# Kernel tuning notes

Hardware: AMD Instinct MI355X
Metric: run time of the kernel (lower is better)

The kernel has to match this reference:

```python
import jax, jax.numpy as jnp
import numpy as np

N, E = 50000, 800000
IN, HID, HEADS = 64, 32, 4


def setup_inputs() -> dict:
    key = jax.random.key(0)
    ks = jax.random.split(key, 18)
    x = jax.random.normal(ks[0], (N, IN), jnp.float32)
    edge_index = jax.random.randint(ks[1], (2, E), 0, N)

    def lin(k, fan_in, fan_out):
        kw, kb = jax.random.split(k)
        bound = 1.0 / np.sqrt(fan_in)
        W = jax.random.uniform(kw, (fan_in, fan_out), jnp.float32, -bound, bound)
        b = jax.random.uniform(kb, (fan_out,), jnp.float32, -bound, bound)
        return W, b

    # layer 1: in=IN, out=HID per head, heads=HEADS, concat=True -> out dim HID*HEADS
    Wq1, bq1 = lin(ks[2], IN, HEADS * HID)
    Wk1, bk1 = lin(ks[3], IN, HEADS * HID)
    Wv1, bv1 = lin(ks[4], IN, HEADS * HID)
    Ws1, bs1 = lin(ks[5], IN, HEADS * HID)  # root/skip lin
    # layer 2: in=HID*HEADS, out=HID, heads=1, concat=False
    IN2 = HID * HEADS
    Wq2, bq2 = lin(ks[6], IN2, HID)
    Wk2, bk2 = lin(ks[7], IN2, HID)
    Wv2, bv2 = lin(ks[8], IN2, HID)
    Ws2, bs2 = lin(ks[9], IN2, HID)
    return dict(x=x, edge_index=edge_index,
                Wq1=Wq1, bq1=bq1, Wk1=Wk1, bk1=bk1, Wv1=Wv1, bv1=bv1, Ws1=Ws1, bs1=bs1,
                Wq2=Wq2, bq2=bq2, Wk2=Wk2, bk2=bk2, Wv2=Wv2, bv2=bv2, Ws2=Ws2, bs2=bs2)


def transformer_conv(x, src, dst, Wq, bq, Wk, bk, Wv, bv, Ws, bs, heads, out_ch, concat):
    """PyG TransformerConv (eval mode, root_weight=True, beta=False)."""
    n = x.shape[0]
    q = (x @ Wq + bq).reshape(n, heads, out_ch)  # [N,H,C]
    k = (x @ Wk + bk).reshape(n, heads, out_ch)
    v = (x @ Wv + bv).reshape(n, heads, out_ch)
    # per-edge attention logits: q_i . k_j / sqrt(C)
    logits = jnp.einsum('ehc,ehc->eh', q[dst], k[src]) / jnp.sqrt(jnp.float32(out_ch))
    # segment softmax over incoming edges of each target node
    m = jax.ops.segment_max(logits, dst, num_segments=n)          # [N,H]
    p = jnp.exp(logits - m[dst])                                   # [E,H]
    denom = jax.ops.segment_sum(p, dst, num_segments=n)            # [N,H]
    alpha = p / denom[dst]                                         # [E,H]
    agg = jax.ops.segment_sum(alpha[:, :, None] * v[src], dst, num_segments=n)  # [N,H,C]
    if concat:
        o = agg.reshape(n, heads * out_ch)
    else:
        o = agg.mean(axis=1)
    return o + x @ Ws + bs


def reference(x, edge_index,
              Wq1, bq1, Wk1, bk1, Wv1, bv1, Ws1, bs1,
              Wq2, bq2, Wk2, bk2, Wv2, bv2, Ws2, bs2):
    src, dst = edge_index[0], edge_index[1]
    h = transformer_conv(x, src, dst, Wq1, bq1, Wk1, bk1, Wv1, bv1, Ws1, bs1,
                         HEADS, HID, True)
    h = jax.nn.elu(h)
    out = transformer_conv(h, src, dst, Wq2, bq2, Wk2, bk2, Wv2, bv2, Ws2, bs2,
                           1, HID, False)
    return out
```

## Files before the change

### kernel.cpp

```cpp
#include <hip/hip_runtime.h>
#include <hip/hip_bf16.h>
#include <hip/hip_fp8.h>

#define N_NODES 50000
#define N_EDGES 800000
#define HB 3125
#define GB1 1563
#define NBS 49

static constexpr float SCALE = 0.17677669529663687f;

typedef __attribute__((ext_vector_type(8))) short bf16x8;
typedef __attribute__((ext_vector_type(4))) float f32x4;
typedef __attribute__((ext_vector_type(2))) float f32x2;
#define MFMA16 __builtin_amdgcn_mfma_f32_16x16x32_bf16
#define CVT8 __builtin_amdgcn_cvt_pk_f32_fp8

static __device__ inline unsigned short f2bf(float f) {
    __hip_bfloat16 h = __float2bfloat16(f);
    return __builtin_bit_cast(unsigned short, h);
}
static __device__ inline unsigned char f2fp8(float f) {
    __hip_fp8_e4m3 h(f);
    return __builtin_bit_cast(unsigned char, h);
}
static __device__ inline f32x2 bfp2(unsigned u) {
    f32x2 r;
    r[0] = __uint_as_float(u << 16);
    r[1] = __uint_as_float(u & 0xffff0000u);
    return r;
}


__global__ __launch_bounds__(256) void k_wf(
    const float* __restrict__ Wq1, const float* __restrict__ Wk1,
    const float* __restrict__ Wv1, const float* __restrict__ Ws1,
    const float* __restrict__ Wq2, const float* __restrict__ Wk2,
    const float* __restrict__ Wv2, const float* __restrict__ Ws2,
    unsigned short* __restrict__ Wf1, unsigned short* __restrict__ Wf2,
    int* __restrict__ cnt)
{
    int id = blockIdx.x * 256 + threadIdx.x;
    if (id < N_NODES + 64) cnt[id] = 0;
    if (id < 32768) {
        int j = id & 7, l = (id >> 3) & 63, ks = (id >> 9) & 1, nt = (id >> 10) & 7, m = (id >> 13) & 3;
        const float* W = (m == 0) ? Wq1 : (m == 1) ? Wk1 : (m == 2) ? Wv1 : Ws1;
        int k = ks * 32 + ((l >> 4) << 3) + j;
        int c = nt * 16 + (l & 15);
        Wf1[id] = f2bf(W[k * 128 + c]);
    } else if (id < 49152) {
        int id2 = id - 32768;
        int j = id2 & 7, l = (id2 >> 3) & 63, ks = (id2 >> 9) & 3, g = (id2 >> 11) & 7;
        int m = g >> 1, t = g & 1;
        const float* W = (m == 0) ? Wq2 : (m == 1) ? Wk2 : (m == 2) ? Wv2 : Ws2;
        int k = ks * 32 + ((l >> 4) << 3) + j;
        int c = t * 16 + (l & 15);
        Wf2[id2] = f2bf(W[k * 32 + c]);
    }
}


__global__ __launch_bounds__(256) void k_hg(
    const int* __restrict__ dst, int* __restrict__ cnt, int* __restrict__ rank,
    const float* __restrict__ x, const unsigned short* __restrict__ Wf1,
    const float* __restrict__ bq, const float* __restrict__ bk,
    const float* __restrict__ bv, const float* __restrict__ bs,
    unsigned short* __restrict__ qs1, unsigned char* __restrict__ kv8, int n)
{
    __shared__ unsigned char smem[4 * 4352];
    if (blockIdx.x < HB) {
        int e = blockIdx.x * 256 + threadIdx.x;
        rank[e] = atomicAdd(&cnt[dst[e]], 1);
        return;
    }
    int w = threadIdx.x >> 6;
    int l = threadIdx.x & 63;
    int rb = (blockIdx.x - HB) * 32;
    int lr = l & 15, lk = l >> 4;
    unsigned short* xs = (unsigned short*)smem;
    {
        int t = threadIdx.x;
        int r = rb + (t >> 3);
        if (r >= n) r = n - 1;
        int c = (t & 7) * 8;
        const float* xp = x + (size_t)r * 64 + c;
        float4 f0 = *(const float4*)xp;
        float4 f1 = *(const float4*)(xp + 4);
        unsigned short* dp = xs + (t >> 3) * 72 + c;
        dp[0] = f2bf(f0.x); dp[1] = f2bf(f0.y); dp[2] = f2bf(f0.z); dp[3] = f2bf(f0.w);
        dp[4] = f2bf(f1.x); dp[5] = f2bf(f1.y); dp[6] = f2bf(f1.z); dp[7] = f2bf(f1.w);
    }
    __syncthreads();
    f32x4 acc[2][8];
#pragma unroll
    for (int mt = 0; mt < 2; ++mt)
#pragma unroll
        for (int nt = 0; nt < 8; ++nt) acc[mt][nt] = (f32x4){0.f, 0.f, 0.f, 0.f};
#pragma unroll
    for (int ks = 0; ks < 2; ++ks) {
        bf16x8 a[2];
#pragma unroll
        for (int mt = 0; mt < 2; ++mt)
            a[mt] = *(const bf16x8*)(xs + (mt * 16 + lr) * 72 + ks * 32 + lk * 8);
#pragma unroll
        for (int nt = 0; nt < 8; ++nt) {
            bf16x8 b = *(const bf16x8*)(Wf1 + (size_t)((w * 8 + nt) * 1024 + ks * 512 + l * 8));
            acc[0][nt] = MFMA16(a[0], b, acc[0][nt], 0, 0, 0);
            acc[1][nt] = MFMA16(a[1], b, acc[1][nt], 0, 0, 0);
        }
    }
    __syncthreads();
    const float* bptr = (w == 0) ? bq : (w == 1) ? bk : (w == 2) ? bv : bs;
    unsigned char* my = smem + w * 4352;
#pragma unroll
    for (int mt = 0; mt < 2; ++mt) {
        if (w == 1 || w == 2) {
            unsigned char* lb = my;
#pragma unroll
            for (int nt = 0; nt < 8; ++nt) {
                float bias = bptr[nt * 16 + lr];
#pragma unroll
                for (int i = 0; i < 4; ++i)
                    lb[(lk * 4 + i) * 144 + nt * 16 + lr] = f2fp8(acc[mt][nt][i] + bias);
            }
            int voff = (w == 2) ? 8 : 0;
#pragma unroll
            for (int p = 0; p < 4; ++p) {
                int rl = p * 4 + lk;
                int r = rb + mt * 16 + rl;
                if (r < n) {
                    uint2 val = *(const uint2*)(lb + rl * 144 + lr * 8);
                    *(uint2*)(kv8 + (size_t)r * 256 + lr * 16 + voff) = val;
                }
            }
        } else {
            unsigned short* ls = (unsigned short*)my;
#pragma unroll
            for (int nt = 0; nt < 8; ++nt) {
                float bias = bptr[nt * 16 + lr];
#pragma unroll
                for (int i = 0; i < 4; ++i)
                    ls[(lk * 4 + i) * 136 + nt * 16 + lr] = f2bf(acc[mt][nt][i] + bias);
            }
            unsigned short* outp = (w == 0) ? qs1 : qs1 + 128;
#pragma unroll
            for (int p = 0; p < 4; ++p) {
                int rl = p * 4 + lk;
                int r = rb + mt * 16 + rl;
                if (r < n) {
                    uint4 val = *(const uint4*)(ls + rl * 136 + lr * 8);
                    *(uint4*)(outp + (size_t)r * 256 + lr * 8) = val;
                }
            }
        }
    }
}


__global__ __launch_bounds__(256) void k_scan(const int* __restrict__ cnt,
                                              int* __restrict__ row,
                                              int* __restrict__ bsum,
                                              int* __restrict__ boff,
                                              int* __restrict__ ctr, int n) {
    __shared__ int wsum[4];
    __shared__ int lastBlk;
    int t = threadIdx.x;
    int base = blockIdx.x * 1024 + t * 4;
    int v0 = (base + 0 < n) ? cnt[base + 0] : 0;
    int v1i = (base + 1 < n) ? cnt[base + 1] : 0;
    int v2 = (base + 2 < n) ? cnt[base + 2] : 0;
    int v3 = (base + 3 < n) ? cnt[base + 3] : 0;
    int s = v0 + v1i + v2 + v3;
    int lane = t & 63, wid = t >> 6;
    int sc = s;
#pragma unroll
    for (int d = 1; d < 64; d <<= 1) {
        int o = __shfl_up(sc, d);
        if (lane >= d) sc += o;
    }
    if (lane == 63) wsum[wid] = sc;
    __syncthreads();
    int woff = 0;
    for (int w = 0; w < wid; ++w) woff += wsum[w];
    int excl = woff + sc - s;
    if (base + 0 < n) row[base + 0] = excl;
    if (base + 1 < n) row[base + 1] = excl + v0;
    if (base + 2 < n) row[base + 2] = excl + v0 + v1i;
    if (base + 3 < n) row[base + 3] = excl + v0 + v1i + v2;
    if (t == 255) {
        bsum[blockIdx.x] = woff + sc;
        __threadfence();
        lastBlk = (atomicAdd(ctr, 1) == NBS - 1);
    }
    __syncthreads();
    if (lastBlk && t < 64) {
        __threadfence();
        int v = (t < NBS) ? ((volatile int*)bsum)[t] : 0;
        int sc2 = v;
#pragma unroll
        for (int d = 1; d < 64; d <<= 1) {
            int o = __shfl_up(sc2, d);
            if (t >= d) sc2 += o;
        }
        boff[t] = sc2 - v;
        if (t == (N_NODES >> 10)) row[N_NODES] = N_EDGES - (sc2 - v);
    }
}


__global__ void k_scat(const int* __restrict__ src, const int* __restrict__ dst,
                       const int* __restrict__ row, const int* __restrict__ boff,
                       const int* __restrict__ rank, int* __restrict__ col) {
    int e = blockIdx.x * 256 + threadIdx.x;
    int de = dst[e];
    col[row[de] + boff[de >> 10] + rank[e]] = src[e];
}


__global__ __launch_bounds__(256) void k_gemm2m(
    const unsigned short* __restrict__ h1b, const unsigned short* __restrict__ Wf2,
    const float* __restrict__ bq, const float* __restrict__ bk,
    const float* __restrict__ bv, const float* __restrict__ bs,
    unsigned short* __restrict__ qs2, unsigned char* __restrict__ k82,
    unsigned short* __restrict__ v2, int n)
{
    __shared__ unsigned short lds[4][32][72];
    int w = threadIdx.x >> 6;
    int l = threadIdx.x & 63;
    int half = w & 1;
    int rb = blockIdx.x * 64 + (w >> 1) * 32;
    int lr = l & 15, lk = l >> 4;
    f32x4 acc[2][4];
#pragma unroll
    for (int mt = 0; mt < 2; ++mt)
#pragma unroll
        for (int nt = 0; nt < 4; ++nt) acc[mt][nt] = (f32x4){0.f, 0.f, 0.f, 0.f};
#pragma unroll
    for (int ks = 0; ks < 4; ++ks) {
        bf16x8 a[2];
#pragma unroll
        for (int mt = 0; mt < 2; ++mt) {
            int r = rb + mt * 16 + lr;
            if (r >= n) r = n - 1;
            a[mt] = *(const bf16x8*)(h1b + (size_t)r * 128 + ks * 32 + lk * 8);
        }
#pragma unroll
        for (int nt = 0; nt < 4; ++nt) {
            int g = half * 4 + nt;
            bf16x8 b = *(const bf16x8*)(Wf2 + (size_t)((g * 4 + ks) * 512 + l * 8));
            acc[0][nt] = MFMA16(a[0], b, acc[0][nt], 0, 0, 0);
            acc[1][nt] = MFMA16(a[1], b, acc[1][nt], 0, 0, 0);
        }
    }
#pragma unroll
    for (int nt = 0; nt < 4; ++nt) {
        int g = half * 4 + nt;
        int mat = g >> 1;
        int c = (g * 16 + lr) & 31;
        const float* bp = (mat == 0) ? bq : (mat == 1) ? bk : (mat == 2) ? bv : bs;
        float bias = bp[c];
#pragma unroll
        for (int mt = 0; mt < 2; ++mt)
#pragma unroll
            for (int i = 0; i < 4; ++i)
                lds[w][mt * 16 + lk * 4 + i][nt * 16 + lr] = f2bf(acc[mt][nt][i] + bias);
    }
    int rl8 = l >> 3, ci = (l & 7) * 4;
#pragma unroll
    for (int p = 0; p < 4; ++p) {
        int rl = p * 8 + rl8;
        int r = rb + rl;
        if (r < n) {
            uint2 va = *(const uint2*)&lds[w][rl][ci];
            uint2 vb = *(const uint2*)&lds[w][rl][32 + ci];
            if (half == 0) {
                *(uint2*)(qs2 + (size_t)r * 64 + ci) = va;
                unsigned pk =
                      (unsigned)f2fp8(__uint_as_float(vb.x << 16))
                    | ((unsigned)f2fp8(__uint_as_float(vb.x & 0xffff0000u)) << 8)
                    | ((unsigned)f2fp8(__uint_as_float(vb.y << 16)) << 16)
                    | ((unsigned)f2fp8(__uint_as_float(vb.y & 0xffff0000u)) << 24);
                *(unsigned*)(k82 + (size_t)r * 32 + ci) = pk;
            } else {
                *(uint2*)(v2 + (size_t)r * 32 + ci) = va;
                *(uint2*)(qs2 + (size_t)r * 64 + 32 + ci) = vb;
            }
        }
    }
}


__global__ __launch_bounds__(256) void k_agg1(
    const unsigned short* __restrict__ qs1, const unsigned char* __restrict__ kv8,
    const int* __restrict__ row, const int* __restrict__ boff,
    const int* __restrict__ col, uint4* __restrict__ h1b, int n)
{
    int i = blockIdx.x * 4 + (threadIdx.x >> 6);
    if (i >= n) return;
    int lane = threadIdx.x & 63;
    int slot = lane >> 4, w = lane & 15;
    f32x2 q2[4];
    {
        uint4 qu = *(const uint4*)(qs1 + (size_t)i * 256 + w * 8);
        q2[0] = bfp2(qu.x); q2[1] = bfp2(qu.y); q2[2] = bfp2(qu.z); q2[3] = bfp2(qu.w);
    }
    f32x2 acc2[4] = {};
    float d = 0.f;
    int s = row[i] + boff[i >> 10];
    int e = row[i + 1] + boff[(i + 1) >> 10];
    for (int t = s; t < e; t += 8) {
        int ta = t + slot, tb = t + 4 + slot;
        bool va = ta < e, vb = tb < e;
        int ja = col[va ? ta : s];
        int jb = col[vb ? tb : s];
        uint4 A = *(const uint4*)(kv8 + (size_t)ja * 256 + w * 16);
        uint4 B = *(const uint4*)(kv8 + (size_t)jb * 256 + w * 16);
        f32x2 pa = CVT8(A.x, false) * q2[0];
        pa += CVT8(A.x, true)  * q2[1];
        pa += CVT8(A.y, false) * q2[2];
        pa += CVT8(A.y, true)  * q2[3];
        f32x2 pb = CVT8(B.x, false) * q2[0];
        pb += CVT8(B.x, true)  * q2[1];
        pb += CVT8(B.y, false) * q2[2];
        pb += CVT8(B.y, true)  * q2[3];
        float la = pa[0] + pa[1];
        float lb = pb[0] + pb[1];
        la += __shfl_xor(la, 1);  lb += __shfl_xor(lb, 1);
        la += __shfl_xor(la, 2);  lb += __shfl_xor(lb, 2);
        float wa = va ? __expf(la * SCALE) : 0.f;
        float wb = vb ? __expf(lb * SCALE) : 0.f;
        d += wa + wb;
        f32x2 wa2 = (f32x2){wa, wa};
        f32x2 wb2 = (f32x2){wb, wb};
        acc2[0] += wa2 * CVT8(A.z, false);
        acc2[1] += wa2 * CVT8(A.z, true);
        acc2[2] += wa2 * CVT8(A.w, false);
        acc2[3] += wa2 * CVT8(A.w, true);
        acc2[0] += wb2 * CVT8(B.z, false);
        acc2[1] += wb2 * CVT8(B.z, true);
        acc2[2] += wb2 * CVT8(B.w, false);
        acc2[3] += wb2 * CVT8(B.w, true);
    }
    float acc[8] = {acc2[0][0], acc2[0][1], acc2[1][0], acc2[1][1],
                    acc2[2][0], acc2[2][1], acc2[3][0], acc2[3][1]};
#pragma unroll
    for (int m = 16; m <= 32; m <<= 1) {
        d += __shfl_xor(d, m);
#pragma unroll
        for (int c = 0; c < 8; ++c) acc[c] += __shfl_xor(acc[c], m);
    }
    if (slot == 0) {
        float inv = (d > 0.f) ? 1.f / d : 0.f;
        uint4 su = *(const uint4*)(qs1 + (size_t)i * 256 + 128 + w * 8);
        f32x2 sv[4] = {bfp2(su.x), bfp2(su.y), bfp2(su.z), bfp2(su.w)};
        unsigned o[4];
#pragma unroll
        for (int p = 0; p < 4; ++p) {
            float rx = acc[2 * p] * inv + sv[p][0];
            float ry = acc[2 * p + 1] * inv + sv[p][1];
            rx = (rx > 0.f) ? rx : expm1f(rx);
            ry = (ry > 0.f) ? ry : expm1f(ry);
            o[p] = ((unsigned)f2bf(ry) << 16) | (unsigned)f2bf(rx);
        }
        h1b[(size_t)i * 16 + w] = make_uint4(o[0], o[1], o[2], o[3]);
    }
}


__global__ __launch_bounds__(256) void k_agg2(
    const unsigned short* __restrict__ qs2, const unsigned char* __restrict__ k82,
    const unsigned short* __restrict__ v2,
    const int* __restrict__ row, const int* __restrict__ boff,
    const int* __restrict__ col, float* __restrict__ out, int n)
{
    int i = blockIdx.x * 4 + (threadIdx.x >> 6);
    if (i >= n) return;
    int lane = threadIdx.x & 63;
    int slot = lane >> 2, qr = lane & 3;
    f32x2 q2[4];
    {
        uint4 qu = *(const uint4*)(qs2 + (size_t)i * 64 + qr * 8);
        q2[0] = bfp2(qu.x); q2[1] = bfp2(qu.y); q2[2] = bfp2(qu.z); q2[3] = bfp2(qu.w);
    }
    f32x2 acc2[4] = {};
    float d = 0.f;
    int s = row[i] + boff[i >> 10];
    int e = row[i + 1] + boff[(i + 1) >> 10];
    for (int t = s; t < e; t += 16) {
        int te = t + slot;
        bool va = te < e;
        int j = col[va ? te : s];
        uint2 ku = *(const uint2*)(k82 + (size_t)j * 32 + qr * 8);
        uint4 vu = *(const uint4*)(v2 + (size_t)j * 32 + qr * 8);
        f32x2 pp = CVT8(ku.x, false) * q2[0];
        pp += CVT8(ku.x, true)  * q2[1];
        pp += CVT8(ku.y, false) * q2[2];
        pp += CVT8(ku.y, true)  * q2[3];
        float lg = pp[0] + pp[1];
        lg += __shfl_xor(lg, 1);
        lg += __shfl_xor(lg, 2);
        float wv = va ? __expf(lg * SCALE) : 0.f;
        d += wv;
        f32x2 w2 = (f32x2){wv, wv};
        acc2[0] += w2 * bfp2(vu.x);
        acc2[1] += w2 * bfp2(vu.y);
        acc2[2] += w2 * bfp2(vu.z);
        acc2[3] += w2 * bfp2(vu.w);
    }
    float acc[8] = {acc2[0][0], acc2[0][1], acc2[1][0], acc2[1][1],
                    acc2[2][0], acc2[2][1], acc2[3][0], acc2[3][1]};
#pragma unroll
    for (int m = 4; m <= 32; m <<= 1) {
        d += __shfl_xor(d, m);
#pragma unroll
        for (int c = 0; c < 8; ++c) acc[c] += __shfl_xor(acc[c], m);
    }
    if (slot == 0) {
        float inv = (d > 0.f) ? 1.f / d : 0.f;
        uint4 su = *(const uint4*)(qs2 + (size_t)i * 64 + 32 + qr * 8);
        f32x2 sv[4] = {bfp2(su.x), bfp2(su.y), bfp2(su.z), bfp2(su.w)};
        float4 o0, o1;
        o0.x = acc[0] * inv + sv[0][0];
        o0.y = acc[1] * inv + sv[0][1];
        o0.z = acc[2] * inv + sv[1][0];
        o0.w = acc[3] * inv + sv[1][1];
        o1.x = acc[4] * inv + sv[2][0];
        o1.y = acc[5] * inv + sv[2][1];
        o1.z = acc[6] * inv + sv[3][0];
        o1.w = acc[7] * inv + sv[3][1];
        *(float4*)&out[(size_t)i * 32 + qr * 8] = o0;
        *(float4*)&out[(size_t)i * 32 + qr * 8 + 4] = o1;
    }
}


extern "C" void kernel_launch(void* const* d_in, const int* in_sizes, int n_in,
                              void* d_out, int out_size, void* d_ws, size_t ws_size,
                              hipStream_t stream)
{
    const int N = N_NODES, E = N_EDGES;
    const float* x   = (const float*)d_in[0];
    const int* edge  = (const int*)d_in[1];
    const int* src   = edge;
    const int* dst   = edge + E;
    const float* Wq1 = (const float*)d_in[2];  const float* bq1 = (const float*)d_in[3];
    const float* Wk1 = (const float*)d_in[4];  const float* bk1 = (const float*)d_in[5];
    const float* Wv1 = (const float*)d_in[6];  const float* bv1 = (const float*)d_in[7];
    const float* Ws1 = (const float*)d_in[8];  const float* bs1 = (const float*)d_in[9];
    const float* Wq2 = (const float*)d_in[10]; const float* bq2 = (const float*)d_in[11];
    const float* Wk2 = (const float*)d_in[12]; const float* bk2 = (const float*)d_in[13];
    const float* Wv2 = (const float*)d_in[14]; const float* bv2 = (const float*)d_in[15];
    const float* Ws2 = (const float*)d_in[16]; const float* bs2 = (const float*)d_in[17];

    char* ws = (char*)d_ws;
    size_t off = 0;
    auto alloc = [&](size_t bytes) -> void* {
        void* p = ws + off;
        off += (bytes + 255) & ~(size_t)255;
        return p;
    };
    unsigned short* qs1 = (unsigned short*)alloc((size_t)N * 256 * 2);
    unsigned char*  kv8 = (unsigned char*)alloc((size_t)N * 256);
    unsigned short* h1b = (unsigned short*)alloc((size_t)N * 128 * 2);
    unsigned short* qs2 = (unsigned short*)alloc((size_t)N * 64 * 2);
    unsigned char*  k82 = (unsigned char*)alloc((size_t)N * 32);
    unsigned short* v2  = (unsigned short*)alloc((size_t)N * 32 * 2);
    unsigned short* Wf1 = (unsigned short*)alloc(32768 * 2);
    unsigned short* Wf2 = (unsigned short*)alloc(16384 * 2);
    int* row_ptr  = (int*)alloc((size_t)(N + 1) * 4);
    int* cnt      = (int*)alloc((size_t)(N + 64) * 4);
    int* ctr      = cnt + N;
    int* rank     = (int*)alloc((size_t)E * 4);
    int* colb     = (int*)alloc((size_t)E * 4);
    int* bsum     = (int*)alloc(64 * 4);
    int* boff     = (int*)alloc(64 * 4);

    int WFB = (N + 64 + 255) / 256;

    k_wf<<<WFB, 256, 0, stream>>>(Wq1, Wk1, Wv1, Ws1, Wq2, Wk2, Wv2, Ws2,
                                  Wf1, Wf2, cnt);
    k_hg<<<HB + GB1, 256, 0, stream>>>(dst, cnt, rank,
                                       x, Wf1, bq1, bk1, bv1, bs1, qs1, kv8, N);
    k_scan<<<NBS, 256, 0, stream>>>(cnt, row_ptr, bsum, boff, ctr, N);
    k_scat<<<HB, 256, 0, stream>>>(src, dst, row_ptr, boff, rank, colb);
    k_agg1<<<(N + 3) / 4, 256, 0, stream>>>(qs1, kv8, row_ptr, boff, colb, (uint4*)h1b, N);
    k_gemm2m<<<(N + 63) / 64, 256, 0, stream>>>(h1b, Wf2, bq2, bk2, bv2, bs2, qs2, k82, v2, N);
    k_agg2<<<(N + 3) / 4, 256, 0, stream>>>(qs2, k82, v2, row_ptr, boff, colb, (float*)d_out, N);
}
```

Before: 154.9 us.

## Split layer-1 projection GEMM across histogram and scatter kernels with 16-row tiles

The layer-1 QKVS projection now runs on 16-row tiles instead of 32-row tiles. About half of the GEMM blocks ride along with the histogram kernel and the other half with the edge-scatter kernel, so the compute-bound GEMM overlaps with the atomic- and scatter-bound CSR building stages. Each tile writes its epilogue in two halves, which shrinks the LDS staging. The bounds checks on rows are gone, which relies on 1562 plus 1563 tiles of 16 rows exactly covering the 50000 nodes.

```diff
diff --git a/kernel.cpp b/kernel.cpp
--- a/kernel.cpp
+++ b/kernel.cpp
@@ -5,7 +5,8 @@
 #define N_NODES 50000
 #define N_EDGES 800000
 #define HB 3125
-#define GB1 1563
+#define GA 1562
+#define GB2 1563
 #define NBS 49
 
 static constexpr float SCALE = 0.17677669529663687f;
@@ -29,6 +30,79 @@
     r[0] = __uint_as_float(u << 16);
     r[1] = __uint_as_float(u & 0xffff0000u);
     return r;
+}
+
+
+static __device__ __forceinline__ void gemm16(
+    int rb, unsigned char* smem,
+    const float* __restrict__ x, const unsigned short* __restrict__ Wf1,
+    const float* __restrict__ bq, const float* __restrict__ bk,
+    const float* __restrict__ bv, const float* __restrict__ bs,
+    unsigned short* __restrict__ qs1, unsigned char* __restrict__ kv8)
+{
+    int w = threadIdx.x >> 6;
+    int l = threadIdx.x & 63;
+    int lr = l & 15, lk = l >> 4;
+    unsigned short* xs = (unsigned short*)smem;
+    unsigned char* ep = smem + 2560;
+    {
+        int row = threadIdx.x >> 4, c = (threadIdx.x & 15) * 4;
+        float4 f = *(const float4*)(x + (size_t)(rb + row) * 64 + c);
+        unsigned short* dp = xs + row * 72 + c;
+        dp[0] = f2bf(f.x); dp[1] = f2bf(f.y); dp[2] = f2bf(f.z); dp[3] = f2bf(f.w);
+    }
+    __syncthreads();
+    bf16x8 a0 = *(const bf16x8*)(xs + lr * 72 + lk * 8);
+    bf16x8 a1 = *(const bf16x8*)(xs + lr * 72 + 32 + lk * 8);
+    const float* bptr = (w == 0) ? bq : (w == 1) ? bk : (w == 2) ? bv : bs;
+#pragma unroll
+    for (int hf = 0; hf < 2; ++hf) {
+        f32x4 acc[4];
+#pragma unroll
+        for (int nt4 = 0; nt4 < 4; ++nt4) acc[nt4] = (f32x4){0.f, 0.f, 0.f, 0.f};
+#pragma unroll
+        for (int nt4 = 0; nt4 < 4; ++nt4) {
+            int nt = hf * 4 + nt4;
+            bf16x8 b0 = *(const bf16x8*)(Wf1 + (size_t)((w * 8 + nt) * 1024) + l * 8);
+            bf16x8 b1 = *(const bf16x8*)(Wf1 + (size_t)((w * 8 + nt) * 1024 + 512) + l * 8);
+            acc[nt4] = MFMA16(a0, b0, acc[nt4], 0, 0, 0);
+            acc[nt4] = MFMA16(a1, b1, acc[nt4], 0, 0, 0);
+        }
+        if (w == 1 || w == 2) {
+            unsigned char* lb = ep + w * 2304;
+#pragma unroll
+            for (int nt4 = 0; nt4 < 4; ++nt4) {
+                float bias = bptr[hf * 64 + nt4 * 16 + lr];
+#pragma unroll
+                for (int i = 0; i < 4; ++i)
+                    lb[(lk * 4 + i) * 72 + nt4 * 16 + lr] = f2fp8(acc[nt4][i] + bias);
+            }
+            int voff = (w == 2) ? 8 : 0;
+            int g = lr & 7, b = lr >> 3;
+#pragma unroll
+            for (int p = 0; p < 2; ++p) {
+                int rl = p * 8 + lk * 2 + b;
+                uint2 val = *(const uint2*)(lb + rl * 72 + g * 8);
+                *(uint2*)(kv8 + (size_t)(rb + rl) * 256 + (hf * 8 + g) * 16 + voff) = val;
+            }
+        } else {
+            unsigned short* ls = (unsigned short*)(ep + w * 2304);
+#pragma unroll
+            for (int nt4 = 0; nt4 < 4; ++nt4) {
+                float bias = bptr[hf * 64 + nt4 * 16 + lr];
+#pragma unroll
+                for (int i = 0; i < 4; ++i)
+                    ls[(lk * 4 + i) * 72 + nt4 * 16 + lr] = f2bf(acc[nt4][i] + bias);
+            }
+            int base = (w == 0) ? 0 : 128;
+#pragma unroll
+            for (int p = 0; p < 4; ++p) {
+                int rl = p * 4 + lk;
+                uint2 val = *(const uint2*)(ls + rl * 72 + lr * 4);
+                *(uint2*)(qs1 + (size_t)(rb + rl) * 256 + base + hf * 64 + lr * 4) = val;
+            }
+        }
+    }
 }
 
 
@@ -60,100 +134,20 @@
 }
 
 
-__global__ __launch_bounds__(256) void k_hg(
+__global__ __launch_bounds__(256) void k_hg2(
     const int* __restrict__ dst, int* __restrict__ cnt, int* __restrict__ rank,
     const float* __restrict__ x, const unsigned short* __restrict__ Wf1,
     const float* __restrict__ bq, const float* __restrict__ bk,
     const float* __restrict__ bv, const float* __restrict__ bs,
-    unsigned short* __restrict__ qs1, unsigned char* __restrict__ kv8, int n)
-{
-    __shared__ unsigned char smem[4 * 4352];
+    unsigned short* __restrict__ qs1, unsigned char* __restrict__ kv8)
+{
+    __shared__ unsigned char smem[2560 + 4 * 2304];
     if (blockIdx.x < HB) {
         int e = blockIdx.x * 256 + threadIdx.x;
         rank[e] = atomicAdd(&cnt[dst[e]], 1);
         return;
     }
-    int w = threadIdx.x >> 6;
-    int l = threadIdx.x & 63;
-    int rb = (blockIdx.x - HB) * 32;
-    int lr = l & 15, lk = l >> 4;
-    unsigned short* xs = (unsigned short*)smem;
-    {
-        int t = threadIdx.x;
-        int r = rb + (t >> 3);
-        if (r >= n) r = n - 1;
-        int c = (t & 7) * 8;
-        const float* xp = x + (size_t)r * 64 + c;
-        float4 f0 = *(const float4*)xp;
-        float4 f1 = *(const float4*)(xp + 4);
-        unsigned short* dp = xs + (t >> 3) * 72 + c;
-        dp[0] = f2bf(f0.x); dp[1] = f2bf(f0.y); dp[2] = f2bf(f0.z); dp[3] = f2bf(f0.w);
-        dp[4] = f2bf(f1.x); dp[5] = f2bf(f1.y); dp[6] = f2bf(f1.z); dp[7] = f2bf(f1.w);
-    }
-    __syncthreads();
-    f32x4 acc[2][8];
-#pragma unroll
-    for (int mt = 0; mt < 2; ++mt)
-#pragma unroll
-        for (int nt = 0; nt < 8; ++nt) acc[mt][nt] = (f32x4){0.f, 0.f, 0.f, 0.f};
-#pragma unroll
-    for (int ks = 0; ks < 2; ++ks) {
-        bf16x8 a[2];
-#pragma unroll
-        for (int mt = 0; mt < 2; ++mt)
-            a[mt] = *(const bf16x8*)(xs + (mt * 16 + lr) * 72 + ks * 32 + lk * 8);
-#pragma unroll
-        for (int nt = 0; nt < 8; ++nt) {
-            bf16x8 b = *(const bf16x8*)(Wf1 + (size_t)((w * 8 + nt) * 1024 + ks * 512 + l * 8));
-            acc[0][nt] = MFMA16(a[0], b, acc[0][nt], 0, 0, 0);
-            acc[1][nt] = MFMA16(a[1], b, acc[1][nt], 0, 0, 0);
-        }
-    }
-    __syncthreads();
-    const float* bptr = (w == 0) ? bq : (w == 1) ? bk : (w == 2) ? bv : bs;
-    unsigned char* my = smem + w * 4352;
-#pragma unroll
-    for (int mt = 0; mt < 2; ++mt) {
-        if (w == 1 || w == 2) {
-            unsigned char* lb = my;
-#pragma unroll
-            for (int nt = 0; nt < 8; ++nt) {
-                float bias = bptr[nt * 16 + lr];
-#pragma unroll
-                for (int i = 0; i < 4; ++i)
-                    lb[(lk * 4 + i) * 144 + nt * 16 + lr] = f2fp8(acc[mt][nt][i] + bias);
-            }
-            int voff = (w == 2) ? 8 : 0;
-#pragma unroll
-            for (int p = 0; p < 4; ++p) {
-                int rl = p * 4 + lk;
-                int r = rb + mt * 16 + rl;
-                if (r < n) {
-                    uint2 val = *(const uint2*)(lb + rl * 144 + lr * 8);
-                    *(uint2*)(kv8 + (size_t)r * 256 + lr * 16 + voff) = val;
-                }
-            }
-        } else {
-            unsigned short* ls = (unsigned short*)my;
-#pragma unroll
-            for (int nt = 0; nt < 8; ++nt) {
-                float bias = bptr[nt * 16 + lr];
-#pragma unroll
-                for (int i = 0; i < 4; ++i)
-                    ls[(lk * 4 + i) * 136 + nt * 16 + lr] = f2bf(acc[mt][nt][i] + bias);
-            }
-            unsigned short* outp = (w == 0) ? qs1 : qs1 + 128;
-#pragma unroll
-            for (int p = 0; p < 4; ++p) {
-                int rl = p * 4 + lk;
-                int r = rb + mt * 16 + rl;
-                if (r < n) {
-                    uint4 val = *(const uint4*)(ls + rl * 136 + lr * 8);
-                    *(uint4*)(outp + (size_t)r * 256 + lr * 8) = val;
-                }
-            }
-        }
-    }
+    gemm16((blockIdx.x - HB) * 16, smem, x, Wf1, bq, bk, bv, bs, qs1, kv8);
 }
 
 
@@ -208,12 +202,23 @@
 }
 
 
-__global__ void k_scat(const int* __restrict__ src, const int* __restrict__ dst,
-                       const int* __restrict__ row, const int* __restrict__ boff,
-                       const int* __restrict__ rank, int* __restrict__ col) {
-    int e = blockIdx.x * 256 + threadIdx.x;
-    int de = dst[e];
-    col[row[de] + boff[de >> 10] + rank[e]] = src[e];
+__global__ __launch_bounds__(256) void k_sg2(
+    const int* __restrict__ src, const int* __restrict__ dst,
+    const int* __restrict__ row, const int* __restrict__ boff,
+    const int* __restrict__ rank, int* __restrict__ col,
+    const float* __restrict__ x, const unsigned short* __restrict__ Wf1,
+    const float* __restrict__ bq, const float* __restrict__ bk,
+    const float* __restrict__ bv, const float* __restrict__ bs,
+    unsigned short* __restrict__ qs1, unsigned char* __restrict__ kv8)
+{
+    __shared__ unsigned char smem[2560 + 4 * 2304];
+    if (blockIdx.x >= GB2) {
+        int e = (blockIdx.x - GB2) * 256 + threadIdx.x;
+        int de = dst[e];
+        col[row[de] + boff[de >> 10] + rank[e]] = src[e];
+        return;
+    }
+    gemm16((GA + blockIdx.x) * 16, smem, x, Wf1, bq, bk, bv, bs, qs1, kv8);
 }
 
 
@@ -479,10 +484,11 @@
 
     k_wf<<<WFB, 256, 0, stream>>>(Wq1, Wk1, Wv1, Ws1, Wq2, Wk2, Wv2, Ws2,
                                   Wf1, Wf2, cnt);
-    k_hg<<<HB + GB1, 256, 0, stream>>>(dst, cnt, rank,
-                                       x, Wf1, bq1, bk1, bv1, bs1, qs1, kv8, N);
+    k_hg2<<<HB + GA, 256, 0, stream>>>(dst, cnt, rank,
+                                       x, Wf1, bq1, bk1, bv1, bs1, qs1, kv8);
     k_scan<<<NBS, 256, 0, stream>>>(cnt, row_ptr, bsum, boff, ctr, N);
-    k_scat<<<HB, 256, 0, stream>>>(src, dst, row_ptr, boff, rank, colb);
+    k_sg2<<<GB2 + HB, 256, 0, stream>>>(src, dst, row_ptr, boff, rank, colb,
+                                        x, Wf1, bq1, bk1, bv1, bs1, qs1, kv8);
     k_agg1<<<(N + 3) / 4, 256, 0, stream>>>(qs1, kv8, row_ptr, boff, colb, (uint4*)h1b, N);
     k_gemm2m<<<(N + 63) / 64, 256, 0, stream>>>(h1b, Wf2, bq2, bk2, bv2, bs2, qs2, k82, v2, N);
     k_agg2<<<(N + 3) / 4, 256, 0, stream>>>(qs2, k82, v2, row_ptr, boff, colb, (float*)d_out, N);
```

Measured after the change: 154.3 us. Within noise of the previous version (-0.4%).
